# Optimization experiments

Hardware: AMD Instinct MI355X
Metric: run time of the kernel (lower is better)

Reference implementation:

```python
import jax, jax.numpy as jnp
import numpy as np

HEIGHT = 32
WIDTH = 32
N = HEIGHT * WIDTH  # 1024 tokens
HEADS = 8
DIM_HEAD = 64
SCALE = DIM_HEAD ** -0.5


def _relative_pos_index_dis(h=HEIGHT, w=WIDTH):
    ch = np.arange(h)
    cw = np.arange(w)
    coords = np.stack(np.meshgrid(ch, cw, indexing='ij'))  # [2,h,w]
    flat = coords.reshape(2, -1)                            # [2,N]
    rel = flat[:, :, None] - flat[:, None, :]               # [2,N,N]
    rel = rel.transpose(1, 2, 0).astype(np.int64)           # [N,N,2]
    dis = (rel[:, :, 0].astype(np.float32) / h) ** 2 + (rel[:, :, 1].astype(np.float32) / w) ** 2
    rel[:, :, 0] += h - 1
    rel[:, :, 1] += w - 1
    rel[:, :, 0] *= 2 * w - 1
    idx = rel.sum(-1)
    return idx, dis

_REL_IDX_NP, _DIS_NP = _relative_pos_index_dis()
REL_IDX = jnp.asarray(_REL_IDX_NP)   # [N,N] int
DIS = jnp.asarray(_DIS_NP)           # [N,N] float32


def setup_inputs() -> dict:
    key = jax.random.key(0)
    k1, k2, k3, k4, k5 = jax.random.split(key, 5)
    dim = 512
    inner = HEADS * DIM_HEAD
    x = jax.random.normal(k1, (8, N, dim), dtype=jnp.float32)
    W_qkv = jax.random.normal(k2, (dim, 3 * inner), dtype=jnp.float32) * (dim ** -0.5)
    W_out = jax.random.normal(k3, (inner, dim), dtype=jnp.float32) * (inner ** -0.5)
    b_out = jnp.zeros((dim,), dtype=jnp.float32)
    rel_bias_table = jax.random.normal(k4, ((2 * HEIGHT - 1) * (2 * WIDTH - 1), HEADS), dtype=jnp.float32) * 0.02
    # torch init: zeros + range(1,heads)*0.1 -> [0.1, 0.2, ..., 0.8]
    headsita = (jnp.arange(1, HEADS + 1, dtype=jnp.float32) * 0.1)
    return {"x": x, "W_qkv": W_qkv, "W_out": W_out, "b_out": b_out,
            "rel_bias_table": rel_bias_table, "headsita": headsita, "rpe": 1}


def reference(x, W_qkv, W_out, b_out, rel_bias_table, headsita, rpe):
    B = x.shape[0]
    qkv = x @ W_qkv                              # [B,N,3*inner]
    q, k, v = jnp.split(qkv, 3, axis=-1)
    def to_heads(t):
        return t.reshape(B, N, HEADS, DIM_HEAD).transpose(0, 2, 1, 3)  # [B,H,N,D]
    q, k, v = to_heads(q), to_heads(k), to_heads(v)
    dots0 = jnp.einsum('bhid,bhjd->bhij', q, k) * SCALE  # [B,H,N,N]
    if rpe:
        # gathered relative-position bias: [N,N,H] -> [H,N,N]
        rel_bias = rel_bias_table[REL_IDX].transpose(2, 0, 1)
        factor = 1.0 / (2.0 * headsita ** 2 + 1e-10)     # [H]
        pos_embed = jnp.exp(-factor[:, None, None] * DIS[None, :, :])  # [H,N,N]
        dots = dots0 + rel_bias[None] + 0.01 * pos_embed[None]
    else:
        dots = dots0
    attn = jax.nn.softmax(dots, axis=-1)
    out = jnp.einsum('bhij,bhjd->bhid', attn, v)          # [B,H,N,D]
    out = out.transpose(0, 2, 1, 3).reshape(B, N, HEADS * DIM_HEAD)
    out = out @ W_out + b_out
    return out, jax.nn.softmax(dots0, axis=-1)
```

## Files before the change

kernel.cpp:

```cpp
#include <hip/hip_runtime.h>
#include <hip/hip_bf16.h>

typedef __attribute__((ext_vector_type(8))) short bf16x8;
typedef __attribute__((ext_vector_type(4))) float f32x4;
typedef float f32x4u __attribute__((ext_vector_type(4), aligned(4)));
typedef __attribute__((ext_vector_type(4))) unsigned int uint32x4;

#define N_TOK 1024
#define HEADS 8
#define DIM_HEAD 64
#define BATCH 8
#define DIMM 512
#define INNER 512
#define QKV_COLS 1536

#define MFMA16 __builtin_amdgcn_mfma_f32_16x16x32_bf16

__device__ inline short f2bf(float f) {
  union { float f; unsigned u; } v;
  v.f = f;
  unsigned r = v.u + 0x7fffu + ((v.u >> 16) & 1u);
  return (short)(r >> 16);
}

__device__ inline unsigned pack2bf(float a, float b) {
  return ((unsigned)(unsigned short)f2bf(a)) | (((unsigned)(unsigned short)f2bf(b)) << 16);
}

__device__ inline void lds_barrier() {
  asm volatile("s_waitcnt lgkmcnt(0)" ::: "memory");
  __builtin_amdgcn_s_barrier();
  asm volatile("" ::: "memory");
}

__device__ inline void gload_lds16(const short* g, short* l) {
  __builtin_amdgcn_global_load_lds(
      (const __attribute__((address_space(1))) void*)g,
      (__attribute__((address_space(3))) void*)l, 16, 0, 0);
}

__global__ __launch_bounds__(256)
void prep_kernel(const float* __restrict__ x, short* __restrict__ xb,
                 const float* __restrict__ Wqkv, short* __restrict__ WqT,
                 const float* __restrict__ Wout, short* __restrict__ WoT,
                 const float* __restrict__ rel, const float* __restrict__ headsita,
                 float* __restrict__ bias2e) {
  const int blk = blockIdx.x, t = threadIdx.x;
  if (blk < 4096) {
    int i = (blk * 256 + t) * 4;
    float4 v = *(const float4*)&x[i];
    short4 o;
    o.x = f2bf(v.x); o.y = f2bf(v.y); o.z = f2bf(v.z); o.w = f2bf(v.w);
    *(short4*)&xb[i] = o;
  } else if (blk < 7168) {
    int id = (blk - 4096) * 256 + t;
    int n = id % 1536, k = id / 1536;
    WqT[n * 512 + k] = f2bf(Wqkv[id]);
  } else if (blk < 8192) {
    int id = (blk - 7168) * 256 + t;
    int n = id & 511, k = id >> 9;
    WoT[n * 512 + k] = f2bf(Wout[id]);
  } else {
    int e = (blk - 8192) * 256 + t;
    int h = e >> 12, idx = e & 4095;
    if (idx >= 3969) return;
    int dr = idx / 63 - 31;
    int dc = idx % 63 - 31;
    float th = headsita[h];
    float factor = 1.f / (2.f * th * th + 1e-10f);
    float dis = (float)(dr * dr + dc * dc) * (1.0f / 1024.0f);
    bias2e[e] = __expf(rel[idx * HEADS + h] + 0.01f * __expf(-factor * dis));
  }
}

template<int SPLIT>
__global__ __launch_bounds__(256)
void gemm_kernel(const short* __restrict__ A, const short* __restrict__ Bt,
                 void* __restrict__ C, const float* __restrict__ bias,
                 short* __restrict__ Qb, short* __restrict__ Kfrag,
                 short* __restrict__ Vfrag,
                 int M, int Nc, int K, int lda)
{
  __shared__ short Ash[128 * 32];
  __shared__ short Bsh[128 * 32];
  const int t = threadIdx.x;
  const int lane = t & 63, wave = t >> 6;
  const int wm = wave >> 1, wn = wave & 1;
  const int m0 = blockIdx.y * 128, n0 = blockIdx.x * 128;
  const int grow = wave * 32 + (lane >> 2);
  const int gcol = (lane & 3) * 8;
  f32x4 acc[4][4] = {};
  for (int k0 = 0; k0 < K; k0 += 32) {
    lds_barrier();
    #pragma unroll
    for (int i = 0; i < 2; ++i) {
      gload_lds16(&A[(size_t)(m0 + grow + i * 16) * lda + k0 + gcol],
                  &Ash[(wave * 32 + i * 16) * 32]);
      gload_lds16(&Bt[(size_t)(n0 + grow + i * 16) * K + k0 + gcol],
                  &Bsh[(wave * 32 + i * 16) * 32]);
    }
    asm volatile("s_waitcnt vmcnt(0)" ::: "memory");
    __builtin_amdgcn_s_barrier();
    asm volatile("" ::: "memory");
    bf16x8 af[4], bfr[4];
    #pragma unroll
    for (int m = 0; m < 4; ++m)
      af[m] = *(const bf16x8*)&Ash[(wm * 64 + m * 16 + (lane & 15)) * 32 + (lane >> 4) * 8];
    #pragma unroll
    for (int n = 0; n < 4; ++n)
      bfr[n] = *(const bf16x8*)&Bsh[(wn * 64 + n * 16 + (lane & 15)) * 32 + (lane >> 4) * 8];
    #pragma unroll
    for (int m = 0; m < 4; ++m)
      #pragma unroll
      for (int n = 0; n < 4; ++n)
        acc[m][n] = MFMA16(af[m], bfr[n], acc[m][n], 0, 0, 0);
  }
  const int r0 = (lane >> 4) * 4, c0 = lane & 15;
  if (!SPLIT) {
    #pragma unroll
    for (int m = 0; m < 4; ++m)
      #pragma unroll
      for (int n = 0; n < 4; ++n) {
        int col = n0 + wn*64 + n*16 + c0;
        float bv = bias[col];
        #pragma unroll
        for (int r = 0; r < 4; ++r) {
          int row = m0 + wm*64 + m*16 + r0 + r;
          ((float*)C)[(size_t)row * Nc + col] = acc[m][n][r] + bv;
        }
      }
  } else {
    const int seg = n0 >> 9;
    #pragma unroll
    for (int m = 0; m < 4; ++m)
      #pragma unroll
      for (int n = 0; n < 4; ++n) {
        const int colg = n0 + wn*64 + n*16 + c0;
        const int rowg0 = m0 + wm*64 + m*16 + r0;
        if (seg == 0) {
          #pragma unroll
          for (int rr = 0; rr < 4; ++rr)
            Qb[(size_t)(rowg0 + rr) * 512 + colg] = f2bf(acc[m][n][rr]);
        } else if (seg == 1) {
          const int d = colg - 512, h = d >> 6, dd = d & 63;
          const int b = rowg0 >> 10, j0 = rowg0 & 1023;
          const size_t base = ((((size_t)(b * 8 + h) * 16 + (j0 >> 6)) * 8)
                               + ((j0 >> 4) & 3) * 2 + (dd >> 5)) * 512
                              + ((dd >> 3) & 3) * 128 + (dd & 7);
          #pragma unroll
          for (int rr = 0; rr < 4; ++rr)
            Kfrag[base + ((j0 + rr) & 15) * 8] = f2bf(acc[m][n][rr]);
        } else {
          const int d = colg - 1024, h = d >> 6, dd = d & 63;
          const int b = rowg0 >> 10, j0 = rowg0 & 1023;
          const int w = j0 >> 7, j7 = j0 & 127;
          const int rgv = (((j7 >> 6) & 1) << 1) | ((j7 >> 3) & 1);
          const int wvv = (j7 >> 4) & 3, e0 = j7 & 7;
          const size_t addr = (((size_t)(b * 8 + h) * 8 + w) * 16 + wvv * 4 + (dd >> 4)) * 512
                              + (rgv * 16 + (dd & 15)) * 8 + e0;
          short4 sv;
          sv.x = f2bf(acc[m][n][0]); sv.y = f2bf(acc[m][n][1]);
          sv.z = f2bf(acc[m][n][2]); sv.w = f2bf(acc[m][n][3]);
          *(short4*)&Vfrag[addr] = sv;
        }
      }
  }
}

__global__ __launch_bounds__(256, 4)
void attn_kernel(short* Qb,
                 const short* __restrict__ Kfrag,
                 const short* __restrict__ Vfrag,
                 const float* __restrict__ bias2e,
                 const int* __restrict__ rpe_p,
                 float* __restrict__ out2)
{
  __shared__ __align__(16) char arena[17408];
  __shared__ float red0[4][16];
  __shared__ float red1[4][16];

  const int t = threadIdx.x;
  const int lane = t & 63, wv = t >> 6;
  const int rg = lane >> 4, cl = lane & 15;

  const int id = blockIdx.x;
  const int bh = (id & 7) * 8 + ((id >> 3) & 7);
  const int i0 = (id >> 6) * 16;
  const int b = bh >> 3, h = bh & 7;
  const size_t rowbase = (size_t)b * N_TOK;

  const size_t qoff = (rowbase + i0 + cl) * 512 + h * DIM_HEAD;
  const bf16x8 qf0 = *(const bf16x8*)&Qb[qoff + rg * 8];
  const bf16x8 qf1 = *(const bf16x8*)&Qb[qoff + 32 + rg * 8];

  const short* kf = Kfrag + (((size_t)bh * 16) * 8 + wv * 2) * 512 + lane * 8;
  f32x4 sc[16];
  bf16x8 a0 = *(const bf16x8*)&kf[0];
  bf16x8 a1 = *(const bf16x8*)&kf[512];
  #pragma unroll
  for (int tj = 0; tj < 16; ++tj) {
    bf16x8 n0, n1;
    if (tj < 15) {
      n0 = *(const bf16x8*)&kf[(tj + 1) * 4096];
      n1 = *(const bf16x8*)&kf[(tj + 1) * 4096 + 512];
    }
    f32x4 z = (f32x4){0.f, 0.f, 0.f, 0.f};
    z = MFMA16(a0, qf0, z, 0, 0, 0);
    z = MFMA16(a1, qf1, z, 0, 0, 0);
    sc[tj] = z;
    a0 = n0; a1 = n1;
  }

  float m = -1e30f;
  #pragma unroll
  for (int tj = 0; tj < 16; ++tj)
    #pragma unroll
    for (int r = 0; r < 4; ++r) m = fmaxf(m, sc[tj][r]);
  m = fmaxf(m, __shfl_xor(m, 16));
  m = fmaxf(m, __shfl_xor(m, 32));
  if (lane < 16) red0[wv][lane] = m;
  lds_barrier();
  m = fmaxf(fmaxf(red0[0][cl], red0[1][cl]), fmaxf(red0[2][cl], red0[3][cl]));

  float s = 0.f;
  #pragma unroll
  for (int tj = 0; tj < 16; ++tj)
    #pragma unroll
    for (int r = 0; r < 4; ++r) {
      float e = __expf((sc[tj][r] - m) * 0.125f);
      sc[tj][r] = e;
      s += e;
    }
  s += __shfl_xor(s, 16);
  s += __shfl_xor(s, 32);
  if (lane < 16) red1[wv][lane] = s;
  lds_barrier();
  const float sm0 = red1[0][cl] + red1[1][cl] + red1[2][cl] + red1[3][cl];
  const float iv0 = 1.f / sm0;

  float* stage = (float*)arena;
  const size_t o2base = ((size_t)(b * HEADS + h) * N_TOK + i0) * N_TOK;
  #pragma unroll
  for (int c = 0; c < 4; ++c) {
    #pragma unroll
    for (int tjl = 0; tjl < 4; ++tjl)
      #pragma unroll
      for (int r = 0; r < 4; ++r)
        stage[(tjl * 64 + wv * 16 + rg * 4 + r) * 17 + cl] = sc[c * 4 + tjl][r] * iv0;
    lds_barrier();
    #pragma unroll
    for (int k = 0; k < 4; ++k) {
      int row = wv * 4 + k;
      #pragma unroll
      for (int e = 0; e < 4; ++e) {
        float v = stage[(e * 64 + lane) * 17 + row];
        out2[o2base + (size_t)row * N_TOK + c * 256 + e * 64 + lane] = v;
      }
    }
    lds_barrier();
  }

  const int i_row = i0 + cl;
  const int ri = i_row >> 5, ci = i_row & 31;
  float iv1;
  if (rpe_p[0]) {
    const float* bt = bias2e + (h << 12);
    const int C = (ri - (wv >> 1)) * 63 + ci - ((wv & 1) * 16 + rg * 4) + 1984;
    float s1 = 0.f;
    #pragma unroll
    for (int tj = 0; tj < 16; ++tj) {
      f32x4u bv = *(const f32x4u*)&bt[C - tj * 126 - 3];
      float v0 = sc[tj][0] * bv[3];
      float v1 = sc[tj][1] * bv[2];
      float v2 = sc[tj][2] * bv[1];
      float v3 = sc[tj][3] * bv[0];
      sc[tj][0] = v0; sc[tj][1] = v1; sc[tj][2] = v2; sc[tj][3] = v3;
      s1 += (v0 + v1) + (v2 + v3);
    }
    s1 += __shfl_xor(s1, 16);
    s1 += __shfl_xor(s1, 32);
    if (lane < 16) red0[wv][lane] = s1;
    lds_barrier();
    iv1 = 1.f / (red0[0][cl] + red0[1][cl] + red0[2][cl] + red0[3][cl]);
  } else {
    iv1 = iv0;
  }

  unsigned short* P_c = (unsigned short*)arena;
  const short* vf = Vfrag + (((size_t)bh * 8) * 16 + wv * 4) * 512 + lane * 8;
  f32x4 oacc[4];
  #pragma unroll
  for (int dt = 0; dt < 4; ++dt) oacc[dt] = (f32x4){0.f, 0.f, 0.f, 0.f};
  #pragma unroll
  for (int ch = 0; ch < 2; ++ch) {
    #pragma unroll
    for (int tj8 = 0; tj8 < 8; ++tj8) {
      int tj = ch * 8 + tj8;
      unsigned u0 = pack2bf(sc[tj][0] * iv1, sc[tj][1] * iv1);
      unsigned u1 = pack2bf(sc[tj][2] * iv1, sc[tj][3] * iv1);
      uint2 uu; uu.x = u0; uu.y = u1;
      *(uint2*)&P_c[cl * 520 + wv * 130 + tj8 * 16 + rg * 4] = uu;
    }
    #pragma unroll
    for (int w4 = 0; w4 < 4; ++w4) {
      int w = ch * 4 + w4;
      int tjr = (2 * w + (rg >> 1)) & 7;
      bf16x8 pb = *(const bf16x8*)&P_c[cl * 520 + wv * 130 + tjr * 16 + (rg & 1) * 8];
      #pragma unroll
      for (int dt = 0; dt < 4; ++dt) {
        bf16x8 va = *(const bf16x8*)&vf[w * 8192 + dt * 512];
        oacc[dt] = MFMA16(va, pb, oacc[dt], 0, 0, 0);
      }
    }
  }

  lds_barrier();
  float* buf = (float*)arena;
  #pragma unroll
  for (int dt = 0; dt < 4; ++dt)
    #pragma unroll
    for (int r = 0; r < 4; ++r)
      buf[wv * 1040 + cl * 65 + dt * 16 + rg * 4 + r] = oacc[dt][r];
  lds_barrier();

  const int i_ = t >> 4, dq = t & 15;
  float o[4];
  #pragma unroll
  for (int k = 0; k < 4; ++k) {
    int d = dq * 4 + k;
    o[k] = buf[0 * 1040 + i_ * 65 + d] + buf[1 * 1040 + i_ * 65 + d]
         + buf[2 * 1040 + i_ * 65 + d] + buf[3 * 1040 + i_ * 65 + d];
  }
  short4 os;
  os.x = f2bf(o[0]); os.y = f2bf(o[1]); os.z = f2bf(o[2]); os.w = f2bf(o[3]);
  *(short4*)&Qb[(rowbase + i0 + i_) * 512 + h * DIM_HEAD + dq * 4] = os;
}

extern "C" void kernel_launch(void* const* d_in, const int* in_sizes, int n_in,
                              void* d_out, int out_size, void* d_ws, size_t ws_size,
                              hipStream_t stream) {
  const float* x    = (const float*)d_in[0];
  const float* Wqkv = (const float*)d_in[1];
  const float* Wout = (const float*)d_in[2];
  const float* bout = (const float*)d_in[3];
  const float* rel  = (const float*)d_in[4];
  const float* sita = (const float*)d_in[5];
  const int*   rpe  = (const int*)d_in[6];

  char* ws = (char*)d_ws;
  short* xb     = (short*)(ws);
  short* WqT    = (short*)(ws + 8388608);
  short* WoT    = (short*)(ws + 9961472);
  short* Qbuf   = (short*)(ws + 10485760);
  short* Kfrag  = (short*)(ws + 18874368);
  float* bias2e = (float*)(ws + 27262976);
  short* Vfrag  = (short*)(ws + 35651584);

  float* out1 = (float*)d_out;
  float* out2 = out1 + (size_t)BATCH * N_TOK * DIMM;

  hipLaunchKernelGGL(prep_kernel, dim3(8320), dim3(256), 0, stream,
                     x, xb, Wqkv, WqT, Wout, WoT, rel, sita, bias2e);
  hipLaunchKernelGGL((gemm_kernel<1>), dim3(12, 64), dim3(256), 0, stream,
                     xb, WqT, (void*)nullptr, (const float*)nullptr,
                     Qbuf, Kfrag, Vfrag, 8192, 1536, 512, 512);
  hipLaunchKernelGGL(attn_kernel, dim3(4096), dim3(256), 0, stream,
                     Qbuf, Kfrag, Vfrag, bias2e, rpe, out2);
  hipLaunchKernelGGL((gemm_kernel<0>), dim3(4, 64), dim3(256), 0, stream,
                     Qbuf, WoT, d_out, bout,
                     (short*)nullptr, (short*)nullptr, (short*)nullptr, 8192, 512, 512, 512);
}
```

Baseline: 158.8 us.

## Tile weight transpose through LDS and deepen K/V prefetch in attention

The weight transpose in the prep kernel now runs as 64x64 tiles staged through shared memory, so both the global reads and the global writes are coalesced and vectorized, replacing the strided scalar stores. This cuts the prep grid from 8320 to 4480 blocks. In the attention kernel, K fragment loads are prefetched two iterations ahead instead of one. V fragment loads are also software-pipelined one step ahead of the PV MFMAs, which raises register pressure and may reduce occupancy.

```diff
diff --git a/kernel.cpp b/kernel.cpp
--- a/kernel.cpp
+++ b/kernel.cpp
@@ -45,6 +45,7 @@
                  const float* __restrict__ Wout, short* __restrict__ WoT,
                  const float* __restrict__ rel, const float* __restrict__ headsita,
                  float* __restrict__ bias2e) {
+  __shared__ short Tt[64][65];
   const int blk = blockIdx.x, t = threadIdx.x;
   if (blk < 4096) {
     int i = (blk * 256 + t) * 4;
@@ -52,16 +53,39 @@
     short4 o;
     o.x = f2bf(v.x); o.y = f2bf(v.y); o.z = f2bf(v.z); o.w = f2bf(v.w);
     *(short4*)&xb[i] = o;
-  } else if (blk < 7168) {
-    int id = (blk - 4096) * 256 + t;
-    int n = id % 1536, k = id / 1536;
-    WqT[n * 512 + k] = f2bf(Wqkv[id]);
-  } else if (blk < 8192) {
-    int id = (blk - 7168) * 256 + t;
-    int n = id & 511, k = id >> 9;
-    WoT[n * 512 + k] = f2bf(Wout[id]);
+  } else if (blk < 4352) {
+    const float* W; short* Wt; int Ncols, kt, nt;
+    if (blk < 4288) {
+      int tt = blk - 4096;
+      W = Wqkv; Wt = WqT; Ncols = 1536; kt = tt / 24; nt = tt % 24;
+    } else {
+      int tt = blk - 4288;
+      W = Wout; Wt = WoT; Ncols = 512; kt = tt >> 3; nt = tt & 7;
+    }
+    {
+      int r = t >> 2, cchunk = (t & 3) * 16;
+      const float* src = &W[(size_t)(kt * 64 + r) * Ncols + nt * 64 + cchunk];
+      #pragma unroll
+      for (int q = 0; q < 4; ++q) {
+        float4 v = *(const float4*)&src[q * 4];
+        Tt[r][cchunk + q*4 + 0] = f2bf(v.x);
+        Tt[r][cchunk + q*4 + 1] = f2bf(v.y);
+        Tt[r][cchunk + q*4 + 2] = f2bf(v.z);
+        Tt[r][cchunk + q*4 + 3] = f2bf(v.w);
+      }
+    }
+    lds_barrier();
+    {
+      int nl = t >> 2, kchunk = (t & 3) * 16;
+      short tmp[16];
+      #pragma unroll
+      for (int j = 0; j < 16; ++j) tmp[j] = Tt[kchunk + j][nl];
+      short* dst = &Wt[(size_t)(nt * 64 + nl) * 512 + kt * 64 + kchunk];
+      *(int4*)&dst[0] = *(int4*)&tmp[0];
+      *(int4*)&dst[8] = *(int4*)&tmp[8];
+    }
   } else {
-    int e = (blk - 8192) * 256 + t;
+    int e = (blk - 4352) * 256 + t;
     int h = e >> 12, idx = e & 4095;
     if (idx >= 3969) return;
     int dr = idx / 63 - 31;
@@ -195,20 +219,24 @@
 
   const short* kf = Kfrag + (((size_t)bh * 16) * 8 + wv * 2) * 512 + lane * 8;
   f32x4 sc[16];
-  bf16x8 a0 = *(const bf16x8*)&kf[0];
-  bf16x8 a1 = *(const bf16x8*)&kf[512];
-  #pragma unroll
-  for (int tj = 0; tj < 16; ++tj) {
-    bf16x8 n0, n1;
-    if (tj < 15) {
-      n0 = *(const bf16x8*)&kf[(tj + 1) * 4096];
-      n1 = *(const bf16x8*)&kf[(tj + 1) * 4096 + 512];
-    }
-    f32x4 z = (f32x4){0.f, 0.f, 0.f, 0.f};
-    z = MFMA16(a0, qf0, z, 0, 0, 0);
-    z = MFMA16(a1, qf1, z, 0, 0, 0);
-    sc[tj] = z;
-    a0 = n0; a1 = n1;
+  {
+    bf16x8 p0a = *(const bf16x8*)&kf[0];
+    bf16x8 p0b = *(const bf16x8*)&kf[512];
+    bf16x8 p1a = *(const bf16x8*)&kf[4096];
+    bf16x8 p1b = *(const bf16x8*)&kf[4096 + 512];
+    #pragma unroll
+    for (int tj = 0; tj < 16; ++tj) {
+      bf16x8 c0 = p0a, c1 = p0b;
+      p0a = p1a; p0b = p1b;
+      if (tj < 14) {
+        p1a = *(const bf16x8*)&kf[(tj + 2) * 4096];
+        p1b = *(const bf16x8*)&kf[(tj + 2) * 4096 + 512];
+      }
+      f32x4 z = (f32x4){0.f, 0.f, 0.f, 0.f};
+      z = MFMA16(c0, qf0, z, 0, 0, 0);
+      z = MFMA16(c1, qf1, z, 0, 0, 0);
+      sc[tj] = z;
+    }
   }
 
   float m = -1e30f;
@@ -263,9 +291,9 @@
   const int i_row = i0 + cl;
   const int ri = i_row >> 5, ci = i_row & 31;
   float iv1;
+  const float* bt = bias2e + (h << 12);
+  const int C = (ri - (wv >> 1)) * 63 + ci - ((wv & 1) * 16 + rg * 4) + 1984;
   if (rpe_p[0]) {
-    const float* bt = bias2e + (h << 12);
-    const int C = (ri - (wv >> 1)) * 63 + ci - ((wv & 1) * 16 + rg * 4) + 1984;
     float s1 = 0.f;
     #pragma unroll
     for (int tj = 0; tj < 16; ++tj) {
@@ -291,6 +319,10 @@
   f32x4 oacc[4];
   #pragma unroll
   for (int dt = 0; dt < 4; ++dt) oacc[dt] = (f32x4){0.f, 0.f, 0.f, 0.f};
+  bf16x8 vc0 = *(const bf16x8*)&vf[0];
+  bf16x8 vc1 = *(const bf16x8*)&vf[512];
+  bf16x8 vc2 = *(const bf16x8*)&vf[1024];
+  bf16x8 vc3 = *(const bf16x8*)&vf[1536];
   #pragma unroll
   for (int ch = 0; ch < 2; ++ch) {
     #pragma unroll
@@ -304,13 +336,20 @@
     #pragma unroll
     for (int w4 = 0; w4 < 4; ++w4) {
       int w = ch * 4 + w4;
+      bf16x8 vn0, vn1, vn2, vn3;
+      if (w < 7) {
+        vn0 = *(const bf16x8*)&vf[(w + 1) * 8192];
+        vn1 = *(const bf16x8*)&vf[(w + 1) * 8192 + 512];
+        vn2 = *(const bf16x8*)&vf[(w + 1) * 8192 + 1024];
+        vn3 = *(const bf16x8*)&vf[(w + 1) * 8192 + 1536];
+      }
       int tjr = (2 * w + (rg >> 1)) & 7;
       bf16x8 pb = *(const bf16x8*)&P_c[cl * 520 + wv * 130 + tjr * 16 + (rg & 1) * 8];
-      #pragma unroll
-      for (int dt = 0; dt < 4; ++dt) {
-        bf16x8 va = *(const bf16x8*)&vf[w * 8192 + dt * 512];
-        oacc[dt] = MFMA16(va, pb, oacc[dt], 0, 0, 0);
-      }
+      oacc[0] = MFMA16(vc0, pb, oacc[0], 0, 0, 0);
+      oacc[1] = MFMA16(vc1, pb, oacc[1], 0, 0, 0);
+      oacc[2] = MFMA16(vc2, pb, oacc[2], 0, 0, 0);
+      oacc[3] = MFMA16(vc3, pb, oacc[3], 0, 0, 0);
+      vc0 = vn0; vc1 = vn1; vc2 = vn2; vc3 = vn3;
     }
   }
 
@@ -359,7 +398,7 @@
   float* out1 = (float*)d_out;
   float* out2 = out1 + (size_t)BATCH * N_TOK * DIMM;
 
-  hipLaunchKernelGGL(prep_kernel, dim3(8320), dim3(256), 0, stream,
+  hipLaunchKernelGGL(prep_kernel, dim3(4480), dim3(256), 0, stream,
                      x, xb, Wqkv, WqT, Wout, WoT, rel, sita, bias2e);
   hipLaunchKernelGGL((gemm_kernel<1>), dim3(12, 64), dim3(256), 0, stream,
                      xb, WqT, (void*)nullptr, (const float*)nullptr,
```

Result: faster. 151.9 us (-4.4%).
